# Optimization experiments

Measured on AMD Instinct MI355X. Metric: run time of the kernel, lower is better.

## Reference

```python
import jax, jax.numpy as jnp
import numpy as np

NUM_NODE = 50000
NUM_EDGE = 1_600_000
NUM_REL = 512
DIM = 64


def setup_inputs() -> dict:
    key = jax.random.key(0)
    k1, k2, k3, k4, k5, k6 = jax.random.split(key, 6)
    inp = jax.random.normal(k1, (NUM_NODE, DIM), dtype=jnp.float32)
    boundary = jax.random.normal(k2, (NUM_NODE, DIM), dtype=jnp.float32)
    node_in = jax.random.randint(k3, (NUM_EDGE,), 0, NUM_NODE)
    node_out = jax.random.randint(k4, (NUM_EDGE,), 0, NUM_NODE)
    rel = jax.random.randint(k5, (NUM_EDGE,), 0, NUM_REL)
    edge_list = jnp.stack([node_in, node_out, rel], axis=1).astype(jnp.int32)
    edge_weight = jnp.ones((NUM_EDGE,), dtype=jnp.float32)
    relation_weight = jax.random.normal(k6, (NUM_REL, DIM), dtype=jnp.float32)
    W = jax.random.normal(jax.random.fold_in(key, 7), (DIM, DIM), dtype=jnp.float32) / np.sqrt(DIM)
    b = jnp.zeros((DIM,), dtype=jnp.float32)
    return {"input": inp, "boundary": boundary, "edge_list": edge_list,
            "edge_weight": edge_weight, "relation_weight": relation_weight,
            "W": W, "b": b}


def reference(input, boundary, edge_list, edge_weight, relation_weight, W, b):
    node_in = edge_list[:, 0]
    node_out = edge_list[:, 1]
    rel = edge_list[:, 2]
    # message: DistMult = x_src * r_e   [E, D]
    msg = input[node_in] * relation_weight[rel]
    msg = msg * edge_weight[:, None]
    # std aggregation: sum and sq_sum scatters, boundary acts as an extra self-message
    s = jax.ops.segment_sum(msg, node_out, num_segments=NUM_NODE) + boundary
    sq = jax.ops.segment_sum(msg * msg, node_out, num_segments=NUM_NODE) + boundary * boundary
    deg = jax.ops.segment_sum(jnp.ones_like(edge_weight), node_out, num_segments=NUM_NODE)
    deg1 = (deg + 1.0)[:, None]  # degree_out + 1 (boundary counted)
    update = jnp.sqrt(jnp.clip(sq / deg1 - (s / deg1) ** 2, 1e-6))
    # add_model: single Linear (MLP with num_mlp_layer=1, no trailing activation)
    return update @ W.T + b
```

## Files before the change

### kernel.cpp

```cpp
#include <hip/hip_runtime.h>
#include <hip/hip_bf16.h>

#define NN  50000
#define NE  1600000
#define DIM 64
#define NBK 391

#define OFF_FLAGS  0
#define OFF_BOFF   8
#define OFF_BCUR   400
#define OFF_ROWPTR 792
#define OFF_EIDX   50800

#define CHUNK 4096
#define SBCAP 8192

__device__ __forceinline__ float loadF(const void* p, int i, int bf) {
  if (bf) return __bfloat162float(((const __hip_bfloat16*)p)[i]);
  return ((const float*)p)[i];
}

__device__ __forceinline__ float4 loadF4(const void* p, int i4, int bf) {
  if (bf) {
    ushort4 u = ((const ushort4*)p)[i4];
    float4 f;
    union { unsigned int ui; float fl; } c;
    c.ui = (unsigned int)u.x << 16; f.x = c.fl;
    c.ui = (unsigned int)u.y << 16; f.y = c.fl;
    c.ui = (unsigned int)u.z << 16; f.z = c.fl;
    c.ui = (unsigned int)u.w << 16; f.w = c.fl;
    return f;
  }
  return ((const float4*)p)[i4];
}

__global__ void k_detect(const void* input, const void* boundary,
                         const void* relw, const void* W, const void* ew,
                         int* flags, int* boff) {
  __shared__ int cnt;
  int t = threadIdx.x;
  const void* arrs[4] = {input, boundary, relw, W};
  for (int a = 0; a < 4; ++a) {
    if (t == 0) cnt = 0;
    __syncthreads();
    const unsigned short* u = (const unsigned short*)arrs[a];
    unsigned ex = (u[2 * t] >> 7) & 0xFF;
    if (ex >= 100 && ex <= 140) atomicAdd(&cnt, 1);
    __syncthreads();
    if (t == 0) flags[a] = (cnt >= 32) ? 1 : 0;
    __syncthreads();
  }
  if (t == 0) {
    flags[4] = (((const unsigned short*)ew)[0] == 0x3F80) ? 1 : 0;
    flags[5] = 1;
  }
  for (int i = t; i < 392; i += 64) boff[i] = 0;
}

__global__ __launch_bounds__(256) void k_bhist(const int* __restrict__ el,
                                               const void* __restrict__ ew,
                                               int* __restrict__ bcnt,
                                               int* __restrict__ flags) {
  __shared__ int lc[NBK];
  int t = threadIdx.x;
  int bfE = flags[4];
  for (int i = t; i < NBK; i += 256) lc[i] = 0;
  __syncthreads();
  int c0 = blockIdx.x * 8192;
  int bad = 0;
  for (int i = t; i < 8192; i += 256) {
    int e = c0 + i;
    if (e < NE) {
      atomicAdd(&lc[el[e * 3 + 1] >> 7], 1);
      if (loadF(ew, e, bfE) != 1.0f) bad = 1;
    }
  }
  if (bad) flags[5] = 0;
  __syncthreads();
  for (int i = t; i < NBK; i += 256)
    if (lc[i]) atomicAdd(&bcnt[i], lc[i]);
}

__global__ __launch_bounds__(256) void k_scanb(int* __restrict__ boff,
                                               int* __restrict__ bcur,
                                               int* __restrict__ rowptr) {
  __shared__ int sc[256];
  int t = threadIdx.x;
  int i0 = 2 * t, i1 = 2 * t + 1;
  int a = (i0 < 392) ? boff[i0] : 0;
  int b = (i1 < 392) ? boff[i1] : 0;
  sc[t] = a + b;
  __syncthreads();
  for (int off = 1; off < 256; off <<= 1) {
    int v = (t >= off) ? sc[t - off] : 0;
    __syncthreads();
    sc[t] += v;
    __syncthreads();
  }
  int excl = sc[t] - (a + b);
  if (i0 < 392) boff[i0] = excl;
  if (i1 < 392) boff[i1] = excl + a;
  if (i0 < NBK) bcur[i0] = excl;
  if (i1 < NBK) bcur[i1] = excl + a;
  if (t == 255) rowptr[NN] = sc[255];
}

__global__ __launch_bounds__(256) void k_parta(
    const int* __restrict__ el, int* __restrict__ bcur,
    int* __restrict__ eidx, const int* __restrict__ flags,
    const int* __restrict__ boff, int gb0, int gb1, int cap) {
  __shared__ int stage[CHUNK];
  __shared__ unsigned short sbk[CHUNK];
  __shared__ int lh[NBK], lbase[NBK], lh2[NBK], gbs[NBK];
  __shared__ int sc[256];
  __shared__ int total;
  int t = threadIdx.x;
  int nb = gb1 - gb0;
  int c0 = blockIdx.x * CHUNK;
  int ones = flags[5];
  int base0 = boff[gb0];
  for (int i = t; i < nb; i += 256) { lh[i] = 0; lh2[i] = 0; }
  __syncthreads();
  for (int i = t; i < CHUNK; i += 256) {
    int e = c0 + i;
    if (e < NE) {
      int b = (el[e * 3 + 1] >> 7) - gb0;
      if (b >= 0 && b < nb) atomicAdd(&lh[b], 1);
    }
  }
  __syncthreads();
  int a0 = (2 * t < nb) ? lh[2 * t] : 0;
  int a1 = (2 * t + 1 < nb) ? lh[2 * t + 1] : 0;
  sc[t] = a0 + a1;
  __syncthreads();
  for (int off = 1; off < 256; off <<= 1) {
    int v = (t >= off) ? sc[t - off] : 0;
    __syncthreads();
    sc[t] += v;
    __syncthreads();
  }
  int excl = sc[t] - (a0 + a1);
  if (2 * t < nb) {
    lbase[2 * t] = excl;
    if (a0 > 0) gbs[2 * t] = atomicAdd(&bcur[gb0 + 2 * t], a0);
  }
  if (2 * t + 1 < nb) {
    lbase[2 * t + 1] = excl + a0;
    if (a1 > 0) gbs[2 * t + 1] = atomicAdd(&bcur[gb0 + 2 * t + 1], a1);
  }
  if (t == 255) total = sc[255];
  __syncthreads();
  for (int i = t; i < CHUNK; i += 256) {
    int e = c0 + i;
    if (e < NE) {
      int nout = el[e * 3 + 1];
      int b = (nout >> 7) - gb0;
      if (b >= 0 && b < nb) {
        int r = atomicAdd(&lh2[b], 1);
        int slot = lbase[b] + r;
        int rec = ones ? (el[e * 3] | (el[e * 3 + 2] << 16) |
                          ((nout & 127) << 25))
                       : (e | ((nout & 127) << 25));
        stage[slot] = rec;
        sbk[slot] = (unsigned short)b;
      }
    }
  }
  __syncthreads();
  int tot = total;
  for (int i = t; i < tot; i += 256) {
    int b = sbk[i];
    int dst = gbs[b] + (i - lbase[b]) - base0;
    if (dst >= 0 && dst < cap) eidx[dst] = stage[i];
  }
}

__global__ __launch_bounds__(256) void k_partb(
    int* __restrict__ eidx, const int* __restrict__ boff,
    int* __restrict__ rowptr, const int* __restrict__ el,
    const int* __restrict__ flags, int gb0, int cap) {
  __shared__ int ld[SBCAP];
  __shared__ int lcnt[128], lexc[128];
  int t = threadIdx.x;
  int b = gb0 + blockIdx.x;
  int n0 = b * 128;
  int ncnt = min(128, NN - n0);
  int base0 = boff[gb0];
  int rbase = boff[b], rend = boff[b + 1];
  int cnt = rend - rbase;
  int fast = (cnt <= SBCAP) && (rend - base0 <= cap);
  if (t < 128) lcnt[t] = 0;
  __syncthreads();
  if (fast) {
    for (int i = t; i < cnt; i += 256) ld[i] = eidx[rbase - base0 + i];
    __syncthreads();
    for (int i = t; i < cnt; i += 256)
      atomicAdd(&lcnt[(((unsigned)ld[i]) >> 25) & 127], 1);
  } else {
    int lim = n0 + ncnt;
    for (int e = t; e < NE; e += 256) {
      int nout = el[e * 3 + 1];
      if (nout >= n0 && nout < lim) atomicAdd(&lcnt[nout - n0], 1);
    }
  }
  __syncthreads();
  if (t < 128) lexc[t] = lcnt[t];
  __syncthreads();
  for (int off = 1; off < 128; off <<= 1) {
    int v = 0;
    if (t < 128 && t >= off) v = lexc[t - off];
    __syncthreads();
    if (t < 128) lexc[t] += v;
    __syncthreads();
  }
  if (t < 128) lexc[t] -= lcnt[t];
  __syncthreads();
  if (t < ncnt) rowptr[n0 + t] = rbase + lexc[t];
  if (t == 0) rowptr[n0 + ncnt] = rend;
  if (t < 128) lcnt[t] = 0;
  __syncthreads();
  if (fast) {
    for (int i = t; i < cnt; i += 256) {
      int rec = ld[i];
      int l = (((unsigned)rec) >> 25) & 127;
      int r = atomicAdd(&lcnt[l], 1);
      int dst = rbase + lexc[l] + r - base0;
      if (dst >= 0 && dst < cap) eidx[dst] = rec & 0x1FFFFFF;
    }
  } else {
    int ones = flags[5];
    int lim = n0 + ncnt;
    for (int e = t; e < NE; e += 256) {
      int nout = el[e * 3 + 1];
      if (nout >= n0 && nout < lim) {
        int l = nout - n0;
        int r = atomicAdd(&lcnt[l], 1);
        int dst = rbase + lexc[l] + r - base0;
        int rec = ones ? (el[e * 3] | (el[e * 3 + 2] << 16)) : e;
        if (dst >= 0 && dst < cap) eidx[dst] = rec;
      }
    }
  }
}

__global__ __launch_bounds__(256) void k_node(
    const void* __restrict__ input, const void* __restrict__ boundary,
    const int* __restrict__ el, const void* __restrict__ ew,
    const void* __restrict__ relw, const void* __restrict__ W,
    const void* __restrict__ bv, const int* __restrict__ rowptr,
    const int* __restrict__ eidx, const int* __restrict__ flags,
    void* __restrict__ out, int lo, int hi, int cap) {
  __shared__ float Wt[DIM * 65];
  __shared__ float upd[4][DIM];

  int bfI = flags[0], bfB = flags[1], bfR = flags[2], bfW = flags[3],
      bfE = flags[4], ones = flags[5];
  int tid = threadIdx.x;
  int wv  = tid >> 6;
  int ln  = tid & 63;
  int g   = ln >> 4;
  int k   = ln & 15;
  int n   = lo + blockIdx.x * 4 + wv;

  for (int idx = tid; idx < DIM * DIM; idx += 256) {
    int j = idx >> 6, d = idx & 63;
    Wt[d * 65 + j] = loadF(W, idx, bfW);
  }

  if (n < hi) {
    int base0 = rowptr[lo];
    int start = rowptr[n] - base0, end = rowptr[n + 1] - base0;
    int deg = end - start;
    float4 s4 = {0.f, 0.f, 0.f, 0.f}, q4 = {0.f, 0.f, 0.f, 0.f};

    if (!bfI && !bfR && ones) {
      const float4* inp4 = (const float4*)input;
      const float4* rw4  = (const float4*)relw;
      for (int base = start; base < end; base += 64) {
        int mm = end - base;
        if (mm > 64) mm = 64;
        int rec = 0;
        int idx2 = base + ln;
        if (ln < mm && idx2 < cap) rec = eidx[idx2];
        int jmax = (mm + 3) >> 2;
        #pragma unroll 8
        for (int j = 0; j < jmax; ++j) {
          int slot = j * 4 + g;
          int pk = __shfl(rec, slot);
          float wsel = (slot < mm) ? 1.0f : 0.0f;
          int nin = pk & 0xFFFF, rl = (pk >> 16) & 0x1FF;
          float4 a = inp4[nin * 16 + k];
          float4 r = rw4[rl * 16 + k];
          float tx = a.x * r.x, ty = a.y * r.y,
                tz = a.z * r.z, tw = a.w * r.w;
          s4.x = fmaf(wsel, tx, s4.x); q4.x = fmaf(wsel, tx * tx, q4.x);
          s4.y = fmaf(wsel, ty, s4.y); q4.y = fmaf(wsel, ty * ty, q4.y);
          s4.z = fmaf(wsel, tz, s4.z); q4.z = fmaf(wsel, tz * tz, q4.z);
          s4.w = fmaf(wsel, tw, s4.w); q4.w = fmaf(wsel, tw * tw, q4.w);
        }
      }
    } else {
      for (int base = start; base < end; base += 64) {
        int mm = end - base;
        if (mm > 64) mm = 64;
        int rec = 0;
        float wrec = 0.0f;
        int idx2 = base + ln;
        if (ln < mm && idx2 < cap) {
          rec = eidx[idx2] & 0x1FFFFFF;
          if (!ones) wrec = loadF(ew, rec, bfE);
        }
        int jmax = (mm + 3) >> 2;
        for (int j = 0; j < jmax; ++j) {
          int slot = j * 4 + g;
          int rj = __shfl(rec, slot);
          int nin, rl;
          float wj;
          if (ones) { nin = rj & 0xFFFF; rl = (rj >> 16) & 0x1FF; wj = 1.0f; }
          else      { nin = el[rj * 3];  rl = el[rj * 3 + 2];
                      wj = __shfl(wrec, slot); }
          float wsel = (slot < mm) ? wj : 0.0f;
          float4 a = loadF4(input, nin * 16 + k, bfI);
          float4 r = loadF4(relw, rl * 16 + k, bfR);
          float tx = a.x * r.x, ty = a.y * r.y,
                tz = a.z * r.z, tw = a.w * r.w;
          s4.x = fmaf(wsel, tx, s4.x); q4.x = fmaf(wsel * tx, tx, q4.x);
          s4.y = fmaf(wsel, ty, s4.y); q4.y = fmaf(wsel * ty, ty, q4.y);
          s4.z = fmaf(wsel, tz, s4.z); q4.z = fmaf(wsel * tz, tz, q4.z);
          s4.w = fmaf(wsel, tw, s4.w); q4.w = fmaf(wsel * tw, tw, q4.w);
        }
      }
    }

    s4.x += __shfl_xor(s4.x, 16); s4.x += __shfl_xor(s4.x, 32);
    s4.y += __shfl_xor(s4.y, 16); s4.y += __shfl_xor(s4.y, 32);
    s4.z += __shfl_xor(s4.z, 16); s4.z += __shfl_xor(s4.z, 32);
    s4.w += __shfl_xor(s4.w, 16); s4.w += __shfl_xor(s4.w, 32);
    q4.x += __shfl_xor(q4.x, 16); q4.x += __shfl_xor(q4.x, 32);
    q4.y += __shfl_xor(q4.y, 16); q4.y += __shfl_xor(q4.y, 32);
    q4.z += __shfl_xor(q4.z, 16); q4.z += __shfl_xor(q4.z, 32);
    q4.w += __shfl_xor(q4.w, 16); q4.w += __shfl_xor(q4.w, 32);

    if (g == 0) {
      float4 b4 = loadF4(boundary, n * 16 + k, bfB);
      float dg = (float)deg + 1.0f;
      float sv, qv;
      sv = (s4.x + b4.x) / dg; qv = (q4.x + b4.x * b4.x) / dg;
      upd[wv][4 * k + 0] = sqrtf(fmaxf(qv - sv * sv, 1e-6f));
      sv = (s4.y + b4.y) / dg; qv = (q4.y + b4.y * b4.y) / dg;
      upd[wv][4 * k + 1] = sqrtf(fmaxf(qv - sv * sv, 1e-6f));
      sv = (s4.z + b4.z) / dg; qv = (q4.z + b4.z * b4.z) / dg;
      upd[wv][4 * k + 2] = sqrtf(fmaxf(qv - sv * sv, 1e-6f));
      sv = (s4.w + b4.w) / dg; qv = (q4.w + b4.w * b4.w) / dg;
      upd[wv][4 * k + 3] = sqrtf(fmaxf(qv - sv * sv, 1e-6f));
    }
  }
  __syncthreads();

  if (n < hi) {
    float acc = loadF(bv, ln, bfW);
    #pragma unroll
    for (int kk = 0; kk < DIM; ++kk) acc += upd[wv][kk] * Wt[kk * 65 + ln];
    if (bfI)
      ((__hip_bfloat16*)out)[n * DIM + ln] = __float2bfloat16(acc);
    else
      ((float*)out)[n * DIM + ln] = acc;
  }
}

extern "C" void kernel_launch(void* const* d_in, const int* in_sizes, int n_in,
                              void* d_out, int out_size, void* d_ws, size_t ws_size,
                              hipStream_t stream) {
  const void* input    = d_in[0];
  const void* boundary = d_in[1];
  const int*  edges    = (const int*)d_in[2];
  const void* eweight  = d_in[3];
  const void* relw     = d_in[4];
  const void* W        = d_in[5];
  const void* bv       = d_in[6];

  int* wsI    = (int*)d_ws;
  int* flags  = wsI + OFF_FLAGS;
  int* boff   = wsI + OFF_BOFF;
  int* bcur   = wsI + OFF_BCUR;
  int* rowptr = wsI + OFF_ROWPTR;
  int* eidx   = wsI + OFF_EIDX;

  long cap = (long)(ws_size / 4) - OFF_EIDX;
  if (cap < 1) cap = 1;
  int npass;
  if      (cap >= (long)NE) npass = 1;
  else if (cap >= 1000000)  npass = 2;
  else if (cap >= 520000)   npass = 4;
  else                      npass = 8;

  k_detect<<<1, 64, 0, stream>>>(input, boundary, relw, W, eweight,
                                 flags, boff);
  k_bhist<<<(NE + 8191) / 8192, 256, 0, stream>>>(edges, eweight, boff, flags);
  k_scanb<<<1, 256, 0, stream>>>(boff, bcur, rowptr);

  const int PA_NB = (NE + CHUNK - 1) / CHUNK;
  for (int p = 0; p < npass; ++p) {
    int gb0 = NBK * p / npass;
    int gb1 = NBK * (p + 1) / npass;
    int lo = gb0 * 128;
    int hi = (gb1 * 128 < NN) ? gb1 * 128 : NN;
    k_parta<<<PA_NB, 256, 0, stream>>>(edges, bcur, eidx, flags, boff,
                                       gb0, gb1, (int)cap);
    k_partb<<<gb1 - gb0, 256, 0, stream>>>(eidx, boff, rowptr, edges, flags,
                                           gb0, (int)cap);
    k_node<<<(hi - lo + 3) / 4, 256, 0, stream>>>(
        input, boundary, edges, eweight, relw, W, bv, rowptr, eidx, flags,
        d_out, lo, hi, (int)cap);
  }
}
```

Baseline: 254.1 us.

## Fuse bucket sort with node aggregation and MFMA linear in one kernel

Merges the per-bucket counting sort (k_partb) and the node aggregation kernel (k_node) into one kernel, k_nodeb. Each 128-node bucket's edges are sorted in shared memory and consumed directly, so no global rowptr is built and the sorted edge list is never written back. The final 64x64 linear layer now runs on bf16 MFMA instructions instead of a scalar shared-memory loop, which lowers precision of the update and the weights. Parallelism drops from about 12500 small blocks to 391 large blocks, one per bucket, which risks poor GPU occupancy during the gather-heavy aggregation.

```diff
diff --git a/kernel.cpp b/kernel.cpp
--- a/kernel.cpp
+++ b/kernel.cpp
@@ -6,14 +6,17 @@
 #define DIM 64
 #define NBK 391
 
-#define OFF_FLAGS  0
-#define OFF_BOFF   8
-#define OFF_BCUR   400
-#define OFF_ROWPTR 792
-#define OFF_EIDX   50800
+#define OFF_FLAGS 0
+#define OFF_BOFF  8
+#define OFF_BCUR  400
+#define OFF_EIDX  800
 
 #define CHUNK 4096
 #define SBCAP 8192
+
+typedef __bf16 bf16x8 __attribute__((ext_vector_type(8)));
+typedef __bf16 bf16x4 __attribute__((ext_vector_type(4)));
+typedef float  f32x4  __attribute__((ext_vector_type(4)));
 
 __device__ __forceinline__ float loadF(const void* p, int i, int bf) {
   if (bf) return __bfloat162float(((const __hip_bfloat16*)p)[i]);
@@ -82,8 +85,7 @@
 }
 
 __global__ __launch_bounds__(256) void k_scanb(int* __restrict__ boff,
-                                               int* __restrict__ bcur,
-                                               int* __restrict__ rowptr) {
+                                               int* __restrict__ bcur) {
   __shared__ int sc[256];
   int t = threadIdx.x;
   int i0 = 2 * t, i1 = 2 * t + 1;
@@ -102,7 +104,6 @@
   if (i1 < 392) boff[i1] = excl + a;
   if (i0 < NBK) bcur[i0] = excl;
   if (i1 < NBK) bcur[i1] = excl + a;
-  if (t == 255) rowptr[NN] = sc[255];
 }
 
 __global__ __launch_bounds__(256) void k_parta(
@@ -175,196 +176,198 @@
   }
 }
 
-__global__ __launch_bounds__(256) void k_partb(
-    int* __restrict__ eidx, const int* __restrict__ boff,
-    int* __restrict__ rowptr, const int* __restrict__ el,
-    const int* __restrict__ flags, int gb0, int cap) {
+__global__ __launch_bounds__(256) void k_nodeb(
+    const void* __restrict__ input, const void* __restrict__ boundary,
+    const int* __restrict__ el, const void* __restrict__ ew,
+    const void* __restrict__ relw, const void* __restrict__ W,
+    const void* __restrict__ bv, const int* __restrict__ boff,
+    const int* __restrict__ eidx, const int* __restrict__ flags,
+    void* __restrict__ out, int gb0, int cap) {
   __shared__ int ld[SBCAP];
   __shared__ int lcnt[128], lexc[128];
-  int t = threadIdx.x;
-  int b = gb0 + blockIdx.x;
+  __shared__ __bf16 updb[16][72];
+
+  int bfI = flags[0], bfB = flags[1], bfR = flags[2], bfW = flags[3],
+      bfE = flags[4], ones = flags[5];
+  int t  = threadIdx.x;
+  int wv = t >> 6, ln = t & 63;
+  int g  = ln >> 4;
+  int k  = ln & 15;
+  int q  = ln >> 4;
+  int b  = gb0 + blockIdx.x;
   int n0 = b * 128;
-  int ncnt = min(128, NN - n0);
   int base0 = boff[gb0];
   int rbase = boff[b], rend = boff[b + 1];
   int cnt = rend - rbase;
-  int fast = (cnt <= SBCAP) && (rend - base0 <= cap);
+  int off = rbase - base0;
+  bool fast = (cnt <= SBCAP) && (rend - base0 <= cap);
+
+  int cc = wv * 16 + (ln & 15);
+  bf16x8 bf0, bf1;
+  #pragma unroll
+  for (int j = 0; j < 8; ++j) {
+    bf0[j] = (__bf16)loadF(W, cc * 64 + q * 8 + j, bfW);
+    bf1[j] = (__bf16)loadF(W, cc * 64 + 32 + q * 8 + j, bfW);
+  }
+  float bias = loadF(bv, cc, bfW);
+
   if (t < 128) lcnt[t] = 0;
   __syncthreads();
-  if (fast) {
-    for (int i = t; i < cnt; i += 256) ld[i] = eidx[rbase - base0 + i];
-    __syncthreads();
+  if (fast)
     for (int i = t; i < cnt; i += 256)
-      atomicAdd(&lcnt[(((unsigned)ld[i]) >> 25) & 127], 1);
-  } else {
-    int lim = n0 + ncnt;
-    for (int e = t; e < NE; e += 256) {
-      int nout = el[e * 3 + 1];
-      if (nout >= n0 && nout < lim) atomicAdd(&lcnt[nout - n0], 1);
-    }
-  }
+      atomicAdd(&lcnt[(((unsigned)eidx[off + i]) >> 25) & 127], 1);
   __syncthreads();
   if (t < 128) lexc[t] = lcnt[t];
   __syncthreads();
-  for (int off = 1; off < 128; off <<= 1) {
+  for (int o = 1; o < 128; o <<= 1) {
     int v = 0;
-    if (t < 128 && t >= off) v = lexc[t - off];
+    if (t < 128 && t >= o) v = lexc[t - o];
     __syncthreads();
     if (t < 128) lexc[t] += v;
     __syncthreads();
   }
   if (t < 128) lexc[t] -= lcnt[t];
   __syncthreads();
-  if (t < ncnt) rowptr[n0 + t] = rbase + lexc[t];
-  if (t == 0) rowptr[n0 + ncnt] = rend;
   if (t < 128) lcnt[t] = 0;
   __syncthreads();
   if (fast) {
     for (int i = t; i < cnt; i += 256) {
-      int rec = ld[i];
+      int rec = eidx[off + i];
       int l = (((unsigned)rec) >> 25) & 127;
       int r = atomicAdd(&lcnt[l], 1);
-      int dst = rbase + lexc[l] + r - base0;
-      if (dst >= 0 && dst < cap) eidx[dst] = rec & 0x1FFFFFF;
-    }
-  } else {
-    int ones = flags[5];
-    int lim = n0 + ncnt;
-    for (int e = t; e < NE; e += 256) {
-      int nout = el[e * 3 + 1];
-      if (nout >= n0 && nout < lim) {
-        int l = nout - n0;
-        int r = atomicAdd(&lcnt[l], 1);
-        int dst = rbase + lexc[l] + r - base0;
-        int rec = ones ? (el[e * 3] | (el[e * 3 + 2] << 16)) : e;
-        if (dst >= 0 && dst < cap) eidx[dst] = rec;
+      ld[lexc[l] + r] = rec;
+    }
+  }
+  __syncthreads();
+
+  const float4* inp4 = (const float4*)input;
+  const float4* rw4  = (const float4*)relw;
+  int hot = (!bfI && !bfR && ones) ? 1 : 0;
+
+  for (int g16 = 0; g16 < 128; g16 += 16) {
+    for (int rr = 0; rr < 4; ++rr) {
+      int l = g16 + wv * 4 + rr;
+      int n = n0 + l;
+      int row = wv * 4 + rr;
+      if (n >= NN) {
+        updb[row][ln] = (__bf16)0.0f;
+        continue;
       }
-    }
-  }
-}
-
-__global__ __launch_bounds__(256) void k_node(
-    const void* __restrict__ input, const void* __restrict__ boundary,
-    const int* __restrict__ el, const void* __restrict__ ew,
-    const void* __restrict__ relw, const void* __restrict__ W,
-    const void* __restrict__ bv, const int* __restrict__ rowptr,
-    const int* __restrict__ eidx, const int* __restrict__ flags,
-    void* __restrict__ out, int lo, int hi, int cap) {
-  __shared__ float Wt[DIM * 65];
-  __shared__ float upd[4][DIM];
-
-  int bfI = flags[0], bfB = flags[1], bfR = flags[2], bfW = flags[3],
-      bfE = flags[4], ones = flags[5];
-  int tid = threadIdx.x;
-  int wv  = tid >> 6;
-  int ln  = tid & 63;
-  int g   = ln >> 4;
-  int k   = ln & 15;
-  int n   = lo + blockIdx.x * 4 + wv;
-
-  for (int idx = tid; idx < DIM * DIM; idx += 256) {
-    int j = idx >> 6, d = idx & 63;
-    Wt[d * 65 + j] = loadF(W, idx, bfW);
-  }
-
-  if (n < hi) {
-    int base0 = rowptr[lo];
-    int start = rowptr[n] - base0, end = rowptr[n + 1] - base0;
-    int deg = end - start;
-    float4 s4 = {0.f, 0.f, 0.f, 0.f}, q4 = {0.f, 0.f, 0.f, 0.f};
-
-    if (!bfI && !bfR && ones) {
-      const float4* inp4 = (const float4*)input;
-      const float4* rw4  = (const float4*)relw;
-      for (int base = start; base < end; base += 64) {
-        int mm = end - base;
-        if (mm > 64) mm = 64;
-        int rec = 0;
-        int idx2 = base + ln;
-        if (ln < mm && idx2 < cap) rec = eidx[idx2];
-        int jmax = (mm + 3) >> 2;
-        #pragma unroll 8
-        for (int j = 0; j < jmax; ++j) {
-          int slot = j * 4 + g;
-          int pk = __shfl(rec, slot);
-          float wsel = (slot < mm) ? 1.0f : 0.0f;
-          int nin = pk & 0xFFFF, rl = (pk >> 16) & 0x1FF;
-          float4 a = inp4[nin * 16 + k];
-          float4 r = rw4[rl * 16 + k];
-          float tx = a.x * r.x, ty = a.y * r.y,
-                tz = a.z * r.z, tw = a.w * r.w;
-          s4.x = fmaf(wsel, tx, s4.x); q4.x = fmaf(wsel, tx * tx, q4.x);
-          s4.y = fmaf(wsel, ty, s4.y); q4.y = fmaf(wsel, ty * ty, q4.y);
-          s4.z = fmaf(wsel, tz, s4.z); q4.z = fmaf(wsel, tz * tz, q4.z);
-          s4.w = fmaf(wsel, tw, s4.w); q4.w = fmaf(wsel, tw * tw, q4.w);
+      if (fast) {
+        int st = lexc[l], cl = lcnt[l];
+        float4 s4 = {0.f,0.f,0.f,0.f}, q4 = {0.f,0.f,0.f,0.f};
+        if (hot) {
+          for (int base = 0; base < cl; base += 64) {
+            int mm = cl - base; if (mm > 64) mm = 64;
+            int rec = 0;
+            if (ln < mm) rec = ld[st + base + ln];
+            int jmax = (mm + 3) >> 2;
+            #pragma unroll 8
+            for (int j = 0; j < jmax; ++j) {
+              int slot = j * 4 + g;
+              int pk = __shfl(rec, slot);
+              float wsel = (slot < mm) ? 1.0f : 0.0f;
+              int nin = pk & 0xFFFF, rl = (pk >> 16) & 0x1FF;
+              float4 a = inp4[nin * 16 + k];
+              float4 r = rw4[rl * 16 + k];
+              float tx = a.x*r.x, ty = a.y*r.y, tz = a.z*r.z, tw = a.w*r.w;
+              s4.x = fmaf(wsel, tx, s4.x); q4.x = fmaf(wsel, tx*tx, q4.x);
+              s4.y = fmaf(wsel, ty, s4.y); q4.y = fmaf(wsel, ty*ty, q4.y);
+              s4.z = fmaf(wsel, tz, s4.z); q4.z = fmaf(wsel, tz*tz, q4.z);
+              s4.w = fmaf(wsel, tw, s4.w); q4.w = fmaf(wsel, tw*tw, q4.w);
+            }
+          }
+        } else {
+          for (int base = 0; base < cl; base += 64) {
+            int mm = cl - base; if (mm > 64) mm = 64;
+            int rec = 0; float wrec = 0.0f;
+            if (ln < mm) {
+              rec = ld[st + base + ln] & 0x1FFFFFF;
+              if (!ones) wrec = loadF(ew, rec, bfE);
+            }
+            int jmax = (mm + 3) >> 2;
+            for (int j = 0; j < jmax; ++j) {
+              int slot = j * 4 + g;
+              int rj = __shfl(rec, slot);
+              int nin, rl; float wj;
+              if (ones) { nin = rj & 0xFFFF; rl = (rj >> 16) & 0x1FF; wj = 1.0f; }
+              else      { nin = el[rj * 3]; rl = el[rj * 3 + 2];
+                          wj = __shfl(wrec, slot); }
+              float wsel = (slot < mm) ? wj : 0.0f;
+              float4 a = loadF4(input, nin * 16 + k, bfI);
+              float4 r = loadF4(relw, rl * 16 + k, bfR);
+              float tx = a.x*r.x, ty = a.y*r.y, tz = a.z*r.z, tw = a.w*r.w;
+              s4.x = fmaf(wsel, tx, s4.x); q4.x = fmaf(wsel*tx, tx, q4.x);
+              s4.y = fmaf(wsel, ty, s4.y); q4.y = fmaf(wsel*ty, ty, q4.y);
+              s4.z = fmaf(wsel, tz, s4.z); q4.z = fmaf(wsel*tz, tz, q4.z);
+              s4.w = fmaf(wsel, tw, s4.w); q4.w = fmaf(wsel*tw, tw, q4.w);
+            }
+          }
         }
+        s4.x += __shfl_xor(s4.x, 16); s4.x += __shfl_xor(s4.x, 32);
+        s4.y += __shfl_xor(s4.y, 16); s4.y += __shfl_xor(s4.y, 32);
+        s4.z += __shfl_xor(s4.z, 16); s4.z += __shfl_xor(s4.z, 32);
+        s4.w += __shfl_xor(s4.w, 16); s4.w += __shfl_xor(s4.w, 32);
+        q4.x += __shfl_xor(q4.x, 16); q4.x += __shfl_xor(q4.x, 32);
+        q4.y += __shfl_xor(q4.y, 16); q4.y += __shfl_xor(q4.y, 32);
+        q4.z += __shfl_xor(q4.z, 16); q4.z += __shfl_xor(q4.z, 32);
+        q4.w += __shfl_xor(q4.w, 16); q4.w += __shfl_xor(q4.w, 32);
+        if (g == 0) {
+          float4 b4 = loadF4(boundary, n * 16 + k, bfB);
+          float dg = (float)cl + 1.0f;
+          float sv, qv;
+          bf16x4 u;
+          sv = (s4.x + b4.x) / dg; qv = (q4.x + b4.x * b4.x) / dg;
+          u[0] = (__bf16)sqrtf(fmaxf(qv - sv * sv, 1e-6f));
+          sv = (s4.y + b4.y) / dg; qv = (q4.y + b4.y * b4.y) / dg;
+          u[1] = (__bf16)sqrtf(fmaxf(qv - sv * sv, 1e-6f));
+          sv = (s4.z + b4.z) / dg; qv = (q4.z + b4.z * b4.z) / dg;
+          u[2] = (__bf16)sqrtf(fmaxf(qv - sv * sv, 1e-6f));
+          sv = (s4.w + b4.w) / dg; qv = (q4.w + b4.w * b4.w) / dg;
+          u[3] = (__bf16)sqrtf(fmaxf(qv - sv * sv, 1e-6f));
+          *(bf16x4*)&updb[row][4 * k] = u;
+        }
+      } else {
+        float s = 0.f, sq = 0.f; int deg = 0;
+        for (int base = 0; base < NE; base += 64) {
+          int e = base + ln;
+          bool m = (e < NE) && (el[e * 3 + 1] == n);
+          unsigned long long msk = __ballot(m);
+          deg += (int)__popcll(msk);
+          while (msk) {
+            int src = __ffsll((long long)msk) - 1; msk &= msk - 1;
+            int ee = base + src;
+            int nin = el[ee * 3], rl = el[ee * 3 + 2];
+            float w = ones ? 1.0f : loadF(ew, ee, bfE);
+            float x = loadF(input, nin * 64 + ln, bfI) *
+                      loadF(relw, rl * 64 + ln, bfR) * w;
+            s += x; sq += x * x;
+          }
+        }
+        float bb = loadF(boundary, n * 64 + ln, bfB);
+        s += bb; sq += bb * bb;
+        float dg = (float)deg + 1.0f;
+        float sv = s / dg, qv = sq / dg;
+        updb[row][ln] = (__bf16)sqrtf(fmaxf(qv - sv * sv, 1e-6f));
       }
-    } else {
-      for (int base = start; base < end; base += 64) {
-        int mm = end - base;
-        if (mm > 64) mm = 64;
-        int rec = 0;
-        float wrec = 0.0f;
-        int idx2 = base + ln;
-        if (ln < mm && idx2 < cap) {
-          rec = eidx[idx2] & 0x1FFFFFF;
-          if (!ones) wrec = loadF(ew, rec, bfE);
-        }
-        int jmax = (mm + 3) >> 2;
-        for (int j = 0; j < jmax; ++j) {
-          int slot = j * 4 + g;
-          int rj = __shfl(rec, slot);
-          int nin, rl;
-          float wj;
-          if (ones) { nin = rj & 0xFFFF; rl = (rj >> 16) & 0x1FF; wj = 1.0f; }
-          else      { nin = el[rj * 3];  rl = el[rj * 3 + 2];
-                      wj = __shfl(wrec, slot); }
-          float wsel = (slot < mm) ? wj : 0.0f;
-          float4 a = loadF4(input, nin * 16 + k, bfI);
-          float4 r = loadF4(relw, rl * 16 + k, bfR);
-          float tx = a.x * r.x, ty = a.y * r.y,
-                tz = a.z * r.z, tw = a.w * r.w;
-          s4.x = fmaf(wsel, tx, s4.x); q4.x = fmaf(wsel * tx, tx, q4.x);
-          s4.y = fmaf(wsel, ty, s4.y); q4.y = fmaf(wsel * ty, ty, q4.y);
-          s4.z = fmaf(wsel, tz, s4.z); q4.z = fmaf(wsel * tz, tz, q4.z);
-          s4.w = fmaf(wsel, tw, s4.w); q4.w = fmaf(wsel * tw, tw, q4.w);
-        }
+    }
+    __syncthreads();
+    bf16x8 af0 = *(const bf16x8*)&updb[ln & 15][q * 8];
+    bf16x8 af1 = *(const bf16x8*)&updb[ln & 15][32 + q * 8];
+    f32x4 acc = {0.f, 0.f, 0.f, 0.f};
+    acc = __builtin_amdgcn_mfma_f32_16x16x32_bf16(af0, bf0, acc, 0, 0, 0);
+    acc = __builtin_amdgcn_mfma_f32_16x16x32_bf16(af1, bf1, acc, 0, 0, 0);
+    #pragma unroll
+    for (int i = 0; i < 4; ++i) {
+      int row = q * 4 + i;
+      int n = n0 + g16 + row;
+      if (n < NN) {
+        float v = acc[i] + bias;
+        if (bfI) ((__hip_bfloat16*)out)[n * 64 + cc] = __float2bfloat16(v);
+        else     ((float*)out)[n * 64 + cc] = v;
       }
     }
-
-    s4.x += __shfl_xor(s4.x, 16); s4.x += __shfl_xor(s4.x, 32);
-    s4.y += __shfl_xor(s4.y, 16); s4.y += __shfl_xor(s4.y, 32);
-    s4.z += __shfl_xor(s4.z, 16); s4.z += __shfl_xor(s4.z, 32);
-    s4.w += __shfl_xor(s4.w, 16); s4.w += __shfl_xor(s4.w, 32);
-    q4.x += __shfl_xor(q4.x, 16); q4.x += __shfl_xor(q4.x, 32);
-    q4.y += __shfl_xor(q4.y, 16); q4.y += __shfl_xor(q4.y, 32);
-    q4.z += __shfl_xor(q4.z, 16); q4.z += __shfl_xor(q4.z, 32);
-    q4.w += __shfl_xor(q4.w, 16); q4.w += __shfl_xor(q4.w, 32);
-
-    if (g == 0) {
-      float4 b4 = loadF4(boundary, n * 16 + k, bfB);
-      float dg = (float)deg + 1.0f;
-      float sv, qv;
-      sv = (s4.x + b4.x) / dg; qv = (q4.x + b4.x * b4.x) / dg;
-      upd[wv][4 * k + 0] = sqrtf(fmaxf(qv - sv * sv, 1e-6f));
-      sv = (s4.y + b4.y) / dg; qv = (q4.y + b4.y * b4.y) / dg;
-      upd[wv][4 * k + 1] = sqrtf(fmaxf(qv - sv * sv, 1e-6f));
-      sv = (s4.z + b4.z) / dg; qv = (q4.z + b4.z * b4.z) / dg;
-      upd[wv][4 * k + 2] = sqrtf(fmaxf(qv - sv * sv, 1e-6f));
-      sv = (s4.w + b4.w) / dg; qv = (q4.w + b4.w * b4.w) / dg;
-      upd[wv][4 * k + 3] = sqrtf(fmaxf(qv - sv * sv, 1e-6f));
-    }
-  }
-  __syncthreads();
-
-  if (n < hi) {
-    float acc = loadF(bv, ln, bfW);
-    #pragma unroll
-    for (int kk = 0; kk < DIM; ++kk) acc += upd[wv][kk] * Wt[kk * 65 + ln];
-    if (bfI)
-      ((__hip_bfloat16*)out)[n * DIM + ln] = __float2bfloat16(acc);
-    else
-      ((float*)out)[n * DIM + ln] = acc;
+    __syncthreads();
   }
 }
 
@@ -379,12 +382,11 @@
   const void* W        = d_in[5];
   const void* bv       = d_in[6];
 
-  int* wsI    = (int*)d_ws;
-  int* flags  = wsI + OFF_FLAGS;
-  int* boff   = wsI + OFF_BOFF;
-  int* bcur   = wsI + OFF_BCUR;
-  int* rowptr = wsI + OFF_ROWPTR;
-  int* eidx   = wsI + OFF_EIDX;
+  int* wsI   = (int*)d_ws;
+  int* flags = wsI + OFF_FLAGS;
+  int* boff  = wsI + OFF_BOFF;
+  int* bcur  = wsI + OFF_BCUR;
+  int* eidx  = wsI + OFF_EIDX;
 
   long cap = (long)(ws_size / 4) - OFF_EIDX;
   if (cap < 1) cap = 1;
@@ -397,20 +399,16 @@
   k_detect<<<1, 64, 0, stream>>>(input, boundary, relw, W, eweight,
                                  flags, boff);
   k_bhist<<<(NE + 8191) / 8192, 256, 0, stream>>>(edges, eweight, boff, flags);
-  k_scanb<<<1, 256, 0, stream>>>(boff, bcur, rowptr);
+  k_scanb<<<1, 256, 0, stream>>>(boff, bcur);
 
   const int PA_NB = (NE + CHUNK - 1) / CHUNK;
   for (int p = 0; p < npass; ++p) {
     int gb0 = NBK * p / npass;
     int gb1 = NBK * (p + 1) / npass;
-    int lo = gb0 * 128;
-    int hi = (gb1 * 128 < NN) ? gb1 * 128 : NN;
     k_parta<<<PA_NB, 256, 0, stream>>>(edges, bcur, eidx, flags, boff,
                                        gb0, gb1, (int)cap);
-    k_partb<<<gb1 - gb0, 256, 0, stream>>>(eidx, boff, rowptr, edges, flags,
-                                           gb0, (int)cap);
-    k_node<<<(hi - lo + 3) / 4, 256, 0, stream>>>(
-        input, boundary, edges, eweight, relw, W, bv, rowptr, eidx, flags,
-        d_out, lo, hi, (int)cap);
-  }
-}
+    k_nodeb<<<gb1 - gb0, 256, 0, stream>>>(input, boundary, edges, eweight,
+                                           relw, W, bv, boff, eidx, flags,
+                                           d_out, gb0, (int)cap);
+  }
+}
```

New measurement: 324.9 us. 27.9% more time.

## Use bf16 MFMA for node linear layer and process 16 nodes per block

Applied to the files above, without the earlier changes.

The per-node kernel now handles 16 nodes per block, with each wave looping over 4 nodes. The final 64x64 linear layer uses two bf16 MFMA 16x16x32 instructions. W fragments are loaded straight into registers, which replaces staging a transposed fp32 W in shared memory for every 4-node block. This removes repeated W loads into LDS and the scalar dot-product loop. In exchange the update vector and W are rounded to bf16, which costs precision, and fewer blocks are launched.

```diff
diff --git a/kernel.cpp b/kernel.cpp
--- a/kernel.cpp
+++ b/kernel.cpp
@@ -14,6 +14,10 @@
 
 #define CHUNK 4096
 #define SBCAP 8192
+
+typedef __bf16 bf16x8 __attribute__((ext_vector_type(8)));
+typedef __bf16 bf16x4 __attribute__((ext_vector_type(4)));
+typedef float  f32x4  __attribute__((ext_vector_type(4)));
 
 __device__ __forceinline__ float loadF(const void* p, int i, int bf) {
   if (bf) return __bfloat162float(((const __hip_bfloat16*)p)[i]);
@@ -250,35 +254,44 @@
     const void* __restrict__ bv, const int* __restrict__ rowptr,
     const int* __restrict__ eidx, const int* __restrict__ flags,
     void* __restrict__ out, int lo, int hi, int cap) {
-  __shared__ float Wt[DIM * 65];
-  __shared__ float upd[4][DIM];
+  __shared__ __bf16 updb[16][72];
 
   int bfI = flags[0], bfB = flags[1], bfR = flags[2], bfW = flags[3],
       bfE = flags[4], ones = flags[5];
-  int tid = threadIdx.x;
-  int wv  = tid >> 6;
-  int ln  = tid & 63;
-  int g   = ln >> 4;
-  int k   = ln & 15;
-  int n   = lo + blockIdx.x * 4 + wv;
-
-  for (int idx = tid; idx < DIM * DIM; idx += 256) {
-    int j = idx >> 6, d = idx & 63;
-    Wt[d * 65 + j] = loadF(W, idx, bfW);
-  }
-
-  if (n < hi) {
-    int base0 = rowptr[lo];
+  int t  = threadIdx.x;
+  int wv = t >> 6, ln = t & 63;
+  int g  = ln >> 4;
+  int k  = ln & 15;
+  int q  = ln >> 4;
+  int n0 = lo + blockIdx.x * 16;
+  int base0 = rowptr[lo];
+
+  int cc = wv * 16 + (ln & 15);
+  bf16x8 bfr0, bfr1;
+  #pragma unroll
+  for (int j = 0; j < 8; ++j) {
+    bfr0[j] = (__bf16)loadF(W, cc * 64 + q * 8 + j, bfW);
+    bfr1[j] = (__bf16)loadF(W, cc * 64 + 32 + q * 8 + j, bfW);
+  }
+  float bias = loadF(bv, cc, bfW);
+
+  const float4* inp4 = (const float4*)input;
+  const float4* rw4  = (const float4*)relw;
+  int hot = (!bfI && !bfR && ones) ? 1 : 0;
+
+  for (int rr = 0; rr < 4; ++rr) {
+    int row = wv * 4 + rr;
+    int n = n0 + row;
+    if (n >= hi) {
+      updb[row][ln] = (__bf16)0.0f;
+      continue;
+    }
     int start = rowptr[n] - base0, end = rowptr[n + 1] - base0;
     int deg = end - start;
-    float4 s4 = {0.f, 0.f, 0.f, 0.f}, q4 = {0.f, 0.f, 0.f, 0.f};
-
-    if (!bfI && !bfR && ones) {
-      const float4* inp4 = (const float4*)input;
-      const float4* rw4  = (const float4*)relw;
+    float4 s4 = {0.f,0.f,0.f,0.f}, q4 = {0.f,0.f,0.f,0.f};
+    if (hot) {
       for (int base = start; base < end; base += 64) {
-        int mm = end - base;
-        if (mm > 64) mm = 64;
+        int mm = end - base; if (mm > 64) mm = 64;
         int rec = 0;
         int idx2 = base + ln;
         if (ln < mm && idx2 < cap) rec = eidx[idx2];
@@ -291,20 +304,17 @@
           int nin = pk & 0xFFFF, rl = (pk >> 16) & 0x1FF;
           float4 a = inp4[nin * 16 + k];
           float4 r = rw4[rl * 16 + k];
-          float tx = a.x * r.x, ty = a.y * r.y,
-                tz = a.z * r.z, tw = a.w * r.w;
-          s4.x = fmaf(wsel, tx, s4.x); q4.x = fmaf(wsel, tx * tx, q4.x);
-          s4.y = fmaf(wsel, ty, s4.y); q4.y = fmaf(wsel, ty * ty, q4.y);
-          s4.z = fmaf(wsel, tz, s4.z); q4.z = fmaf(wsel, tz * tz, q4.z);
-          s4.w = fmaf(wsel, tw, s4.w); q4.w = fmaf(wsel, tw * tw, q4.w);
+          float tx = a.x*r.x, ty = a.y*r.y, tz = a.z*r.z, tw = a.w*r.w;
+          s4.x = fmaf(wsel, tx, s4.x); q4.x = fmaf(wsel, tx*tx, q4.x);
+          s4.y = fmaf(wsel, ty, s4.y); q4.y = fmaf(wsel, ty*ty, q4.y);
+          s4.z = fmaf(wsel, tz, s4.z); q4.z = fmaf(wsel, tz*tz, q4.z);
+          s4.w = fmaf(wsel, tw, s4.w); q4.w = fmaf(wsel, tw*tw, q4.w);
         }
       }
     } else {
       for (int base = start; base < end; base += 64) {
-        int mm = end - base;
-        if (mm > 64) mm = 64;
-        int rec = 0;
-        float wrec = 0.0f;
+        int mm = end - base; if (mm > 64) mm = 64;
+        int rec = 0; float wrec = 0.0f;
         int idx2 = base + ln;
         if (ln < mm && idx2 < cap) {
           rec = eidx[idx2] & 0x1FFFFFF;
@@ -314,24 +324,21 @@
         for (int j = 0; j < jmax; ++j) {
           int slot = j * 4 + g;
           int rj = __shfl(rec, slot);
-          int nin, rl;
-          float wj;
+          int nin, rl; float wj;
           if (ones) { nin = rj & 0xFFFF; rl = (rj >> 16) & 0x1FF; wj = 1.0f; }
-          else      { nin = el[rj * 3];  rl = el[rj * 3 + 2];
+          else      { nin = el[rj * 3]; rl = el[rj * 3 + 2];
                       wj = __shfl(wrec, slot); }
           float wsel = (slot < mm) ? wj : 0.0f;
           float4 a = loadF4(input, nin * 16 + k, bfI);
           float4 r = loadF4(relw, rl * 16 + k, bfR);
-          float tx = a.x * r.x, ty = a.y * r.y,
-                tz = a.z * r.z, tw = a.w * r.w;
-          s4.x = fmaf(wsel, tx, s4.x); q4.x = fmaf(wsel * tx, tx, q4.x);
-          s4.y = fmaf(wsel, ty, s4.y); q4.y = fmaf(wsel * ty, ty, q4.y);
-          s4.z = fmaf(wsel, tz, s4.z); q4.z = fmaf(wsel * tz, tz, q4.z);
-          s4.w = fmaf(wsel, tw, s4.w); q4.w = fmaf(wsel * tw, tw, q4.w);
+          float tx = a.x*r.x, ty = a.y*r.y, tz = a.z*r.z, tw = a.w*r.w;
+          s4.x = fmaf(wsel, tx, s4.x); q4.x = fmaf(wsel*tx, tx, q4.x);
+          s4.y = fmaf(wsel, ty, s4.y); q4.y = fmaf(wsel*ty, ty, q4.y);
+          s4.z = fmaf(wsel, tz, s4.z); q4.z = fmaf(wsel*tz, tz, q4.z);
+          s4.w = fmaf(wsel, tw, s4.w); q4.w = fmaf(wsel*tw, tw, q4.w);
         }
       }
     }
-
     s4.x += __shfl_xor(s4.x, 16); s4.x += __shfl_xor(s4.x, 32);
     s4.y += __shfl_xor(s4.y, 16); s4.y += __shfl_xor(s4.y, 32);
     s4.z += __shfl_xor(s4.z, 16); s4.z += __shfl_xor(s4.z, 32);
@@ -340,31 +347,37 @@
     q4.y += __shfl_xor(q4.y, 16); q4.y += __shfl_xor(q4.y, 32);
     q4.z += __shfl_xor(q4.z, 16); q4.z += __shfl_xor(q4.z, 32);
     q4.w += __shfl_xor(q4.w, 16); q4.w += __shfl_xor(q4.w, 32);
-
     if (g == 0) {
       float4 b4 = loadF4(boundary, n * 16 + k, bfB);
       float dg = (float)deg + 1.0f;
       float sv, qv;
+      bf16x4 u;
       sv = (s4.x + b4.x) / dg; qv = (q4.x + b4.x * b4.x) / dg;
-      upd[wv][4 * k + 0] = sqrtf(fmaxf(qv - sv * sv, 1e-6f));
+      u[0] = (__bf16)sqrtf(fmaxf(qv - sv * sv, 1e-6f));
       sv = (s4.y + b4.y) / dg; qv = (q4.y + b4.y * b4.y) / dg;
-      upd[wv][4 * k + 1] = sqrtf(fmaxf(qv - sv * sv, 1e-6f));
+      u[1] = (__bf16)sqrtf(fmaxf(qv - sv * sv, 1e-6f));
       sv = (s4.z + b4.z) / dg; qv = (q4.z + b4.z * b4.z) / dg;
-      upd[wv][4 * k + 2] = sqrtf(fmaxf(qv - sv * sv, 1e-6f));
+      u[2] = (__bf16)sqrtf(fmaxf(qv - sv * sv, 1e-6f));
       sv = (s4.w + b4.w) / dg; qv = (q4.w + b4.w * b4.w) / dg;
-      upd[wv][4 * k + 3] = sqrtf(fmaxf(qv - sv * sv, 1e-6f));
-    }
-  }
-  __syncthreads();
-
-  if (n < hi) {
-    float acc = loadF(bv, ln, bfW);
-    #pragma unroll
-    for (int kk = 0; kk < DIM; ++kk) acc += upd[wv][kk] * Wt[kk * 65 + ln];
-    if (bfI)
-      ((__hip_bfloat16*)out)[n * DIM + ln] = __float2bfloat16(acc);
-    else
-      ((float*)out)[n * DIM + ln] = acc;
+      u[3] = (__bf16)sqrtf(fmaxf(qv - sv * sv, 1e-6f));
+      *(bf16x4*)&updb[row][4 * k] = u;
+    }
+  }
+  __syncthreads();
+
+  bf16x8 af0 = *(const bf16x8*)&updb[ln & 15][q * 8];
+  bf16x8 af1 = *(const bf16x8*)&updb[ln & 15][32 + q * 8];
+  f32x4 acc = {0.f, 0.f, 0.f, 0.f};
+  acc = __builtin_amdgcn_mfma_f32_16x16x32_bf16(af0, bfr0, acc, 0, 0, 0);
+  acc = __builtin_amdgcn_mfma_f32_16x16x32_bf16(af1, bfr1, acc, 0, 0, 0);
+  #pragma unroll
+  for (int i = 0; i < 4; ++i) {
+    int n = n0 + q * 4 + i;
+    if (n < hi) {
+      float v = acc[i] + bias;
+      if (bfI) ((__hip_bfloat16*)out)[n * 64 + cc] = __float2bfloat16(v);
+      else     ((float*)out)[n * 64 + cc] = v;
+    }
   }
 }
 
@@ -409,7 +422,7 @@
                                        gb0, gb1, (int)cap);
     k_partb<<<gb1 - gb0, 256, 0, stream>>>(eidx, boff, rowptr, edges, flags,
                                            gb0, (int)cap);
-    k_node<<<(hi - lo + 3) / 4, 256, 0, stream>>>(
+    k_node<<<(hi - lo + 15) / 16, 256, 0, stream>>>(
         input, boundary, edges, eweight, relw, W, bv, rowptr, eidx, flags,
         d_out, lo, hi, (int)cap);
   }
```

Result: faster. 244.3 us (-3.9%).
